# Optimization experiments

Measured on AMD Instinct MI355X. Metric: run time of the kernel, lower is better.

## Reference

```python
import jax, jax.numpy as jnp
import numpy as np

D_MODEL = 1024
NHEAD = 8
DPH = D_MODEL // NHEAD
DFF = 2048
EPS = 1e-5


def _layernorm(x, w, b):
    mu = jnp.mean(x, axis=-1, keepdims=True)
    var = jnp.mean((x - mu) ** 2, axis=-1, keepdims=True)
    return (x - mu) / jnp.sqrt(var + EPS) * w + b


def setup_inputs() -> dict:
    key = jax.random.key(0)
    ks = jax.random.split(key, 8)
    B, L = 8, 2048
    x = jax.random.normal(ks[0], (B, L, D_MODEL), dtype=jnp.float32)
    # HeadWiseLinear: per-head weight (nhead, dph, 4*dph), bias (nhead, 4*dph)
    ih_w = jax.random.normal(ks[1], (NHEAD, DPH, 4 * DPH), dtype=jnp.float32) * (1.0 / np.sqrt(DPH))
    # forget-gate bias init: linspace(3,6,d_model) in the f slot (second chunk), zeros elsewhere
    init_vals = jnp.linspace(3.0, 6.0, D_MODEL, dtype=jnp.float32).reshape(NHEAD, 1, DPH)
    init_vals = jnp.pad(init_vals, ((0, 0), (1, 2), (0, 0)))  # rows: i, f, z, o
    ih_b = init_vals.reshape(NHEAD, 4 * DPH)
    # linear_hh: Linear(dph, 4*dph, bias=False), stored as (dph, 4*dph) (x @ W)
    hh_w = jax.random.normal(ks[2], (DPH, 4 * DPH), dtype=jnp.float32) * (1.0 / np.sqrt(DPH))
    ln1_w = jnp.ones((D_MODEL,), jnp.float32); ln1_b = jnp.zeros((D_MODEL,), jnp.float32)
    ln2_w = jnp.ones((D_MODEL,), jnp.float32); ln2_b = jnp.zeros((D_MODEL,), jnp.float32)
    hn_w = jnp.ones((DPH,), jnp.float32); hn_b = jnp.zeros((DPH,), jnp.float32)
    ff_w1 = jax.random.normal(ks[3], (D_MODEL, 2 * DFF), dtype=jnp.float32) * (1.0 / np.sqrt(D_MODEL))
    ff_b1 = jnp.zeros((2 * DFF,), jnp.float32)
    ff_w2 = jax.random.normal(ks[4], (DFF, D_MODEL), dtype=jnp.float32) * (1.0 / np.sqrt(DFF))
    ff_b2 = jnp.zeros((D_MODEL,), jnp.float32)
    return dict(x=x, ih_w=ih_w, ih_b=ih_b, hh_w=hh_w, ln1_w=ln1_w, ln1_b=ln1_b,
                hn_w=hn_w, hn_b=hn_b, ln2_w=ln2_w, ln2_b=ln2_b,
                ff_w1=ff_w1, ff_b1=ff_b1, ff_w2=ff_w2, ff_b2=ff_b2)


def _slstm_core(x, ih_w, ih_b, hh_w, hn_w, hn_b):
    B, L, D = x.shape
    xh = x.reshape(B, L, NHEAD, DPH)
    # headwise input projection: (B,L,H,4*dph)
    proj = jnp.einsum('blhd,hdf->blhf', xh, ih_w) + ih_b
    proj = jnp.transpose(proj, (1, 0, 2, 3))  # (L,B,H,4*dph)

    h0 = jnp.zeros((B, NHEAD, DPH), x.dtype)
    c0 = jnp.zeros_like(h0)
    m0 = jnp.full_like(h0, -jnp.inf)  # stabilizer; matches scalar-0 first-step semantics
    n0 = jnp.zeros_like(h0)

    def step(carry, p_t):
        h, c, m, n = carry
        p = p_t + jnp.einsum('bhd,df->bhf', h, hh_w)
        i, f, z, o = jnp.split(p, 4, axis=-1)
        z = jnp.tanh(z)
        o = jax.nn.sigmoid(o)
        f = jax.nn.log_sigmoid(f) + m
        m_new = jnp.maximum(f, i)
        i_s = jnp.exp(i - m_new)
        f_s = jnp.exp(f - m_new)
        c = f_s * c + i_s * z
        n = f_s * n + i_s
        h = o * (c / n)
        return (h, c, m_new, n), h

    (h, c, _, _), out = jax.lax.scan(step, (h0, c0, m0, n0), proj)
    out = jnp.transpose(out, (1, 0, 2, 3))  # (B,L,H,dph)
    out = _layernorm(out, hn_w, hn_b)
    return out.reshape(B, L, D), (h, c)


def reference(x, ih_w, ih_b, hh_w, ln1_w, ln1_b, hn_w, hn_b, ln2_w, ln2_b,
              ff_w1, ff_b1, ff_w2, ff_b2):
    core_out, _ = _slstm_core(_layernorm(x, ln1_w, ln1_b), ih_w, ih_b, hh_w, hn_w, hn_b)
    y = core_out + x
    z = _layernorm(y, ln2_w, ln2_b)
    x12 = z @ ff_w1 + ff_b1
    x1, x2 = jnp.split(x12, 2, axis=-1)
    ff = (x1 * jax.nn.gelu(x2, approximate=False)) @ ff_w2 + ff_b2
    return ff + y
```

## Files before the change

kernel.cpp:

```cpp
#include <hip/hip_runtime.h>
#include <math.h>


#define D_MODEL 1024
#define NHEAD   8
#define DPH     128
#define DFF     2048
#define BATCH   8
#define SEQ     2048
#define NROWS   (BATCH * SEQ)
#define CHUNK_L 256
#define TGRP    32
#define ROWCH   8192
#define LN_EPS  1e-5f

typedef __attribute__((ext_vector_type(8))) short short8;
typedef __attribute__((ext_vector_type(4))) float f32x4;
typedef __attribute__((ext_vector_type(2))) _Float16 h2f;
typedef __attribute__((ext_vector_type(8))) _Float16 h8f;
union H8U { h8f v; h2f p[4]; };

#if __has_builtin(__builtin_amdgcn_fdot2)
#define DOT2(a, b, c) __builtin_amdgcn_fdot2((a), (b), (c), false)
#else
__device__ __forceinline__ float DOT2(h2f a, h2f b, float c) {
  return c + (float)a.x * (float)b.x + (float)a.y * (float)b.y;
}
#endif

__device__ __forceinline__ float qxor1(float v) {
#if __has_builtin(__builtin_amdgcn_update_dpp)
  union { float f; int i; } u; u.f = v;
  u.i = __builtin_amdgcn_update_dpp(u.i, u.i, 0xB1, 0xf, 0xf, true);
  return u.f;
#else
  return __shfl_xor(v, 1, 64);
#endif
}
__device__ __forceinline__ float qxor2(float v) {
#if __has_builtin(__builtin_amdgcn_update_dpp)
  union { float f; int i; } u; u.f = v;
  u.i = __builtin_amdgcn_update_dpp(u.i, u.i, 0x4E, 0xf, 0xf, true);
  return u.f;
#else
  return __shfl_xor(v, 2, 64);
#endif
}

__device__ __forceinline__ void gll16(const float* src, float* lds_base, int lane) {
#if __has_builtin(__builtin_amdgcn_global_load_lds)
  __builtin_amdgcn_global_load_lds(
      (const __attribute__((address_space(1))) unsigned int*)src,
      (__attribute__((address_space(3))) unsigned int*)lds_base, 16, 0, 0);
#else
  *(float4*)((char*)lds_base + lane * 16) = *(const float4*)src;
#endif
}

__device__ __forceinline__ float gelu_exact(float x) {
  return 0.5f * x * (1.0f + erff(x * 0.70710678118654752440f));
}

__device__ __forceinline__ unsigned short f2bf(float f) {
  union { float f; unsigned int u; } v; v.f = f;
  unsigned int r = v.u + 0x7fffu + ((v.u >> 16) & 1u);
  return (unsigned short)(r >> 16);
}

__device__ __forceinline__ float gate_step(float iv, float fv, float zraw, float oraw,
                                           float& c, float& nrm, float& m) {
  const float zv = 1.0f - 2.0f / (__expf(2.0f * zraw) + 1.0f);
  const float ov = 1.0f / (1.0f + __expf(-oraw));
  const float lf = fminf(fv, 0.0f) - __logf(1.0f + __expf(-fabsf(fv)));
  const float ft = lf + m;
  const float mn = fmaxf(ft, iv);
  const float is = __expf(iv - mn);
  const float fs = __expf(ft - mn);
  c = fs * c + is * zv;
  nrm = fs * nrm + is;
  m = mn;
  return ov * (c / nrm);
}

__global__ __launch_bounds__(256) void ln_stats_kernel(
    const float* __restrict__ in, float* __restrict__ mu_out,
    float* __restrict__ rs_out) {
  const int row = blockIdx.x, tid = threadIdx.x;
  const float4 v = ((const float4*)(in + (size_t)row * D_MODEL))[tid];
  float s  = v.x + v.y + v.z + v.w;
  float s2 = v.x*v.x + v.y*v.y + v.z*v.z + v.w*v.w;
  #pragma unroll
  for (int m = 1; m < 64; m <<= 1) { s += __shfl_xor(s, m, 64); s2 += __shfl_xor(s2, m, 64); }
  __shared__ float sa[4], sb[4];
  if ((tid & 63) == 0) { sa[tid >> 6] = s; sb[tid >> 6] = s2; }
  __syncthreads();
  if (tid == 0) {
    const float S  = sa[0] + sa[1] + sa[2] + sa[3];
    const float S2 = sb[0] + sb[1] + sb[2] + sb[3];
    const float mu = S * (1.0f / D_MODEL);
    const float var = S2 * (1.0f / D_MODEL) - mu * mu;
    mu_out[row] = mu;
    rs_out[row] = rsqrtf(var + LN_EPS);
  }
}

__global__ __launch_bounds__(256) void cvt_w(
    const float* __restrict__ src, short* __restrict__ dst, int K, int N) {
  __shared__ float tile[64][68];
  const int n0 = blockIdx.x * 64;
  const int k0 = blockIdx.y * 64;
  const int tid = threadIdx.x;
  #pragma unroll
  for (int i = 0; i < 16; ++i) {
    const int e = i * 256 + tid;
    const int kk = e >> 6, nn = e & 63;
    tile[kk][nn] = src[(size_t)(k0 + kk) * N + n0 + nn];
  }
  __syncthreads();
  #pragma unroll
  for (int i = 0; i < 2; ++i) {
    const int e = i * 256 + tid;
    const int nn = e >> 3, kc = (e & 7) * 8;
    short8 s;
    #pragma unroll
    for (int j = 0; j < 8; ++j) s[j] = (short)f2bf(tile[kc + j][nn]);
    *(short8*)(dst + (size_t)(n0 + nn) * K + k0 + kc) = s;
  }
}

__global__ __launch_bounds__(256) void cvt_hh(
    const float* __restrict__ hhw, h2f* __restrict__ hh2) {
  const int idx = blockIdx.x * 256 + threadIdx.x;
  const int k2 = idx >> 9, j = idx & 511;
  h2f v;
  v.x = (_Float16)hhw[(size_t)(2 * k2) * 512 + j];
  v.y = (_Float16)hhw[(size_t)(2 * k2 + 1) * 512 + j];
  hh2[idx] = v;
}

__global__ __launch_bounds__(256) void proj_gemm(
    const float* __restrict__ x, const float* __restrict__ mu1,
    const float* __restrict__ rs1, const float* __restrict__ ln1w,
    const float* __restrict__ ln1b, const float* __restrict__ ihw,
    const float* __restrict__ ihb, float* __restrict__ proj, int l0) {
  __shared__ __align__(16) float As[64][68];
  __shared__ __align__(16) float Bs[64][128];
  const int h  = blockIdx.z;
  const int n0 = blockIdx.y * 128;
  const int m0 = blockIdx.x * 64;
  const int tid = threadIdx.x;
  const int tm = (tid >> 5) << 3;
  const int tn = (tid & 31) << 2;
  float acc[8][4] = {};
  const float* Bb = ihw + (size_t)h * DPH * 512;
  for (int k0 = 0; k0 < DPH; k0 += 64) {
    #pragma unroll
    for (int i = 0; i < 4; ++i) {
      int idx = tid + i * 256;
      int r = idx >> 4, kk = (idx & 15) << 2;
      const int rowm = m0 + r;
      const int l = l0 + (rowm >> 3), b = rowm & 7;
      const int grow = b * SEQ + l;
      const float4 v = *(const float4*)(x + (size_t)grow * D_MODEL + h * DPH + k0 + kk);
      const float mu = mu1[grow], rs = rs1[grow];
      const float4 wv = *(const float4*)(ln1w + h * DPH + k0 + kk);
      const float4 bv = *(const float4*)(ln1b + h * DPH + k0 + kk);
      float4 o;
      o.x = (v.x - mu) * rs * wv.x + bv.x;
      o.y = (v.y - mu) * rs * wv.y + bv.y;
      o.z = (v.z - mu) * rs * wv.z + bv.z;
      o.w = (v.w - mu) * rs * wv.w + bv.w;
      *(float4*)&As[r][kk] = o;
    }
    #pragma unroll
    for (int i = 0; i < 8; ++i) {
      int idx = tid + i * 256;
      int kk = idx >> 5, nn = (idx & 31) << 2;
      *(float4*)&Bs[kk][nn] = *(const float4*)(Bb + (size_t)(k0 + kk) * 512 + n0 + nn);
    }
    __syncthreads();
    #pragma unroll 4
    for (int kk = 0; kk < 64; ++kk) {
      float a[8];
      #pragma unroll
      for (int i = 0; i < 8; ++i) a[i] = As[tm + i][kk];
      const float4 bv = *(const float4*)&Bs[kk][tn];
      #pragma unroll
      for (int i = 0; i < 8; ++i) {
        acc[i][0] += a[i] * bv.x; acc[i][1] += a[i] * bv.y;
        acc[i][2] += a[i] * bv.z; acc[i][3] += a[i] * bv.w;
      }
    }
    __syncthreads();
  }
  const float4 bias = *(const float4*)(ihb + h * 512 + n0 + tn);
  #pragma unroll
  for (int i = 0; i < 8; ++i) {
    const int rowm = m0 + tm + i;
    float4 o;
    o.x = acc[i][0] + bias.x; o.y = acc[i][1] + bias.y;
    o.z = acc[i][2] + bias.z; o.w = acc[i][3] + bias.w;
    *(float4*)(proj + ((size_t)rowm * NHEAD + h) * 512 + n0 + tn) = o;
  }
}

__global__ __launch_bounds__(512, 1) void scan_chunk(
    const float* __restrict__ proj, const h2f* __restrict__ hh2,
    float* __restrict__ state, float* __restrict__ hout, int l0) {
  const int bh = blockIdx.x, b = bh >> 3, h = bh & 7;
  const int tid = threadIdx.x;
  const int l = tid & 63, w = tid >> 6;
  const int q = l & 3, p = l >> 2;
  const int ch = 16 * w + p;
  __shared__ __align__(16) _Float16 h16[2][128];
  __shared__ __align__(16) float pbuf[2][TGRP][512];
  __shared__ __align__(16) float hstage[TGRP][128];

  h2f w2[4][16];
  #pragma unroll
  for (int j = 0; j < 4; ++j)
    #pragma unroll
    for (int kk = 0; kk < 16; ++kk)
      w2[j][kk] = hh2[(size_t)(16 * q + kk) * 512 + j * 128 + ch];

  float c, nrm, m;
  if (l0 == 0) {
    c = 0.0f; nrm = 0.0f; m = -1e30f;
    if (q == 0 && w == 0) { h16[0][p] = (_Float16)0.0f; }
    if (q == 0) h16[0][ch] = (_Float16)0.0f;
  } else {
    c   = state[bh * 128 + ch];
    nrm = state[8192  + bh * 128 + ch];
    m   = state[16384 + bh * 128 + ch];
    if (q == 0) h16[0][ch] = (_Float16)state[24576 + bh * 128 + ch];
  }

  const float* pbase = proj + (size_t)bh * 512;

  #define STAGE(NB, GR)                                                        \
    {                                                                          \
      _Pragma("unroll")                                                        \
      for (int i = 0; i < 8; ++i) {                                            \
        const int hr = i * 8 + w;                                              \
        const float* src = pbase + (size_t)((GR) * TGRP + (hr >> 1)) * 32768   \
                           + (hr & 1) * 256 + l * 4;                           \
        float* dst = &pbuf[NB][0][0] + hr * 256;                               \
        gll16(src, dst, l);                                                    \
      }                                                                        \
    }

  STAGE(0, 0)
  asm volatile("s_waitcnt vmcnt(0)" ::: "memory");
  __syncthreads();

  float hv = 0.0f;
  for (int t = 0; t < CHUNK_L; ++t) {
    const int tl = t & (TGRP - 1), gb = (t >> 5) & 1, cur = t & 1;
    if (tl == 0 && t + TGRP < CHUNK_L) STAGE(gb ^ 1, (t >> 5) + 1)
    float pa0 = 0.0f, pa1 = 0.0f, pa2 = 0.0f, pa3 = 0.0f;
    {
      const h8f* hp = (const h8f*)&h16[cur][q * 32];
      #pragma unroll
      for (int i = 0; i < 4; ++i) {
        H8U u; u.v = hp[i];
        #pragma unroll
        for (int e = 0; e < 4; ++e) {
          const int kk = i * 4 + e;
          pa0 = DOT2(u.p[e], w2[0][kk], pa0);
          pa1 = DOT2(u.p[e], w2[1][kk], pa1);
          pa2 = DOT2(u.p[e], w2[2][kk], pa2);
          pa3 = DOT2(u.p[e], w2[3][kk], pa3);
        }
      }
    }
    const float pv = pbuf[gb][tl][q * 128 + ch];
    pa0 += (q == 0) ? pv : 0.0f;
    pa1 += (q == 1) ? pv : 0.0f;
    pa2 += (q == 2) ? pv : 0.0f;
    pa3 += (q == 3) ? pv : 0.0f;
    pa0 += qxor1(pa0); pa1 += qxor1(pa1); pa2 += qxor1(pa2); pa3 += qxor1(pa3);
    pa0 += qxor2(pa0); pa1 += qxor2(pa1); pa2 += qxor2(pa2); pa3 += qxor2(pa3);
    hv = gate_step(pa0, pa1, pa2, pa3, c, nrm, m);
    if (q == 0) {
      h16[cur ^ 1][ch] = (_Float16)hv;
      hstage[tl][ch] = hv;
    }
    __syncthreads();
    if (tl == TGRP - 1) {
      const int s = tid >> 4, c8 = (tid & 15) << 3;
      const float4 v0 = *(const float4*)&hstage[s][c8];
      const float4 v1 = *(const float4*)&hstage[s][c8 + 4];
      float* dstp = hout + ((size_t)(b * SEQ + l0 + (t & ~(TGRP - 1)) + s)) * D_MODEL
                    + h * DPH + c8;
      *(float4*)dstp = v0;
      *(float4*)(dstp + 4) = v1;
      __syncthreads();
    }
  }

  if (q == 0) {
    state[bh * 128 + ch]          = c;
    state[8192  + bh * 128 + ch]  = nrm;
    state[16384 + bh * 128 + ch]  = m;
    state[24576 + bh * 128 + ch]  = hv;
  }
  #undef STAGE
}

__global__ __launch_bounds__(256) void post_kernel(
    float* __restrict__ yio, const float* __restrict__ x,
    const float* __restrict__ hnw, const float* __restrict__ hnb,
    float* __restrict__ mu2, float* __restrict__ rs2) {
  const int row = blockIdx.x, tid = threadIdx.x;
  const float4 hv = ((const float4*)(yio + (size_t)row * D_MODEL))[tid];
  float s  = hv.x + hv.y + hv.z + hv.w;
  float s2 = hv.x*hv.x + hv.y*hv.y + hv.z*hv.z + hv.w*hv.w;
  #pragma unroll
  for (int mm = 1; mm < 32; mm <<= 1) {
    s  += __shfl_xor(s,  mm, 32);
    s2 += __shfl_xor(s2, mm, 32);
  }
  const float mu = s * (1.0f / DPH);
  const float var = s2 * (1.0f / DPH) - mu * mu;
  const float rstd = rsqrtf(var + LN_EPS);
  const int dq = tid & 31;
  const float4 w4 = ((const float4*)hnw)[dq];
  const float4 b4 = ((const float4*)hnb)[dq];
  const float4 xv = ((const float4*)(x + (size_t)row * D_MODEL))[tid];
  float4 yv;
  yv.x = (hv.x - mu) * rstd * w4.x + b4.x + xv.x;
  yv.y = (hv.y - mu) * rstd * w4.y + b4.y + xv.y;
  yv.z = (hv.z - mu) * rstd * w4.z + b4.z + xv.z;
  yv.w = (hv.w - mu) * rstd * w4.w + b4.w + xv.w;
  ((float4*)(yio + (size_t)row * D_MODEL))[tid] = yv;
  float t1 = yv.x + yv.y + yv.z + yv.w;
  float t2 = yv.x*yv.x + yv.y*yv.y + yv.z*yv.z + yv.w*yv.w;
  #pragma unroll
  for (int mm = 1; mm < 64; mm <<= 1) {
    t1 += __shfl_xor(t1, mm, 64);
    t2 += __shfl_xor(t2, mm, 64);
  }
  __shared__ float sa[4], sb[4];
  if ((tid & 63) == 0) { sa[tid >> 6] = t1; sb[tid >> 6] = t2; }
  __syncthreads();
  if (tid == 0) {
    const float S  = sa[0] + sa[1] + sa[2] + sa[3];
    const float S2 = sb[0] + sb[1] + sb[2] + sb[3];
    const float m2 = S * (1.0f / D_MODEL);
    const float v2 = S2 * (1.0f / D_MODEL) - m2 * m2;
    mu2[row] = m2;
    rs2[row] = rsqrtf(v2 + LN_EPS);
  }
}

__global__ __launch_bounds__(256) void ff1_gemm(
    const float* __restrict__ y, const float* __restrict__ mu2,
    const float* __restrict__ rs2, const float* __restrict__ ln2w,
    const float* __restrict__ ln2b, const short* __restrict__ w1b,
    const float* __restrict__ b1, short* __restrict__ g, int row0) {
  __shared__ short As[128 * 64];
  __shared__ short Bs1[128 * 64];
  __shared__ short Bs2[128 * 64];
  const int tid = threadIdx.x;
  const int m0 = blockIdx.x * 128;
  const int n0 = blockIdx.y * 128;
  const int lane = tid & 63;
  const int wid = tid >> 6, wr = wid >> 1, wc = wid & 1;
  f32x4 acc1[4][4], acc2[4][4];
  #pragma unroll
  for (int i = 0; i < 4; ++i)
    #pragma unroll
    for (int j = 0; j < 4; ++j) { acc1[i][j] = (f32x4)0.0f; acc2[i][j] = (f32x4)0.0f; }
  for (int k0 = 0; k0 < D_MODEL; k0 += 64) {
    #pragma unroll
    for (int i = 0; i < 4; ++i) {
      const int cidx = tid + i * 256;
      const int r = cidx >> 3, c8 = cidx & 7;
      const int grow = row0 + m0 + r;
      const float* src = y + (size_t)grow * D_MODEL + k0 + c8 * 8;
      const float4 v0 = *(const float4*)src;
      const float4 v1 = *(const float4*)(src + 4);
      const float mu = mu2[grow], rs = rs2[grow];
      const float4 w0 = *(const float4*)(ln2w + k0 + c8 * 8);
      const float4 w1 = *(const float4*)(ln2w + k0 + c8 * 8 + 4);
      const float4 bb0 = *(const float4*)(ln2b + k0 + c8 * 8);
      const float4 bb1 = *(const float4*)(ln2b + k0 + c8 * 8 + 4);
      short8 s;
      s[0] = (short)f2bf((v0.x - mu) * rs * w0.x + bb0.x);
      s[1] = (short)f2bf((v0.y - mu) * rs * w0.y + bb0.y);
      s[2] = (short)f2bf((v0.z - mu) * rs * w0.z + bb0.z);
      s[3] = (short)f2bf((v0.w - mu) * rs * w0.w + bb0.w);
      s[4] = (short)f2bf((v1.x - mu) * rs * w1.x + bb1.x);
      s[5] = (short)f2bf((v1.y - mu) * rs * w1.y + bb1.y);
      s[6] = (short)f2bf((v1.z - mu) * rs * w1.z + bb1.z);
      s[7] = (short)f2bf((v1.w - mu) * rs * w1.w + bb1.w);
      *(short8*)&As[r * 64 + ((c8 ^ (r & 7)) << 3)] = s;
    }
    #pragma unroll
    for (int i = 0; i < 4; ++i) {
      const int cidx = tid + i * 256;
      const int r = cidx >> 3, c8 = cidx & 7;
      const short8 sv1 = *(const short8*)(w1b + (size_t)(n0 + r) * D_MODEL + k0 + c8 * 8);
      const short8 sv2 = *(const short8*)(w1b + (size_t)(DFF + n0 + r) * D_MODEL + k0 + c8 * 8);
      const int off = r * 64 + ((c8 ^ (r & 7)) << 3);
      *(short8*)&Bs1[off] = sv1;
      *(short8*)&Bs2[off] = sv2;
    }
    __syncthreads();
    #pragma unroll
    for (int ks = 0; ks < 2; ++ks) {
      short8 af[4], b1f[4], b2f[4];
      #pragma unroll
      for (int mf = 0; mf < 4; ++mf) {
        const int row = wr * 64 + mf * 16 + (lane & 15);
        const int c8 = ks * 4 + (lane >> 4);
        af[mf] = *(const short8*)&As[row * 64 + ((c8 ^ (row & 7)) << 3)];
      }
      #pragma unroll
      for (int nf = 0; nf < 4; ++nf) {
        const int row = wc * 64 + nf * 16 + (lane & 15);
        const int c8 = ks * 4 + (lane >> 4);
        const int off = row * 64 + ((c8 ^ (row & 7)) << 3);
        b1f[nf] = *(const short8*)&Bs1[off];
        b2f[nf] = *(const short8*)&Bs2[off];
      }
      #pragma unroll
      for (int mf = 0; mf < 4; ++mf)
        #pragma unroll
        for (int nf = 0; nf < 4; ++nf) {
          acc1[mf][nf] = __builtin_amdgcn_mfma_f32_16x16x32_bf16(af[mf], b1f[nf], acc1[mf][nf], 0, 0, 0);
          acc2[mf][nf] = __builtin_amdgcn_mfma_f32_16x16x32_bf16(af[mf], b2f[nf], acc2[mf][nf], 0, 0, 0);
        }
    }
    __syncthreads();
  }
  #pragma unroll
  for (int nf = 0; nf < 4; ++nf) {
    const int col = n0 + wc * 64 + nf * 16 + (lane & 15);
    const float bx1 = b1[col], bx2 = b1[DFF + col];
    #pragma unroll
    for (int mf = 0; mf < 4; ++mf) {
      const int rbase = m0 + wr * 64 + mf * 16 + ((lane >> 4) << 2);
      #pragma unroll
      for (int rr = 0; rr < 4; ++rr) {
        const float x1 = acc1[mf][nf][rr] + bx1;
        const float x2 = acc2[mf][nf][rr] + bx2;
        g[(size_t)(rbase + rr) * DFF + col] = (short)f2bf(x1 * gelu_exact(x2));
      }
    }
  }
}

__global__ __launch_bounds__(256) void ff2_gemm(
    const short* __restrict__ g, const short* __restrict__ w2b,
    const float* __restrict__ b2, float* __restrict__ out, int row0) {
  __shared__ short As[128 * 64];
  __shared__ short Bs[128 * 64];
  const int tid = threadIdx.x;
  const int m0 = blockIdx.x * 128;
  const int n0 = blockIdx.y * 128;
  const int lane = tid & 63;
  const int wid = tid >> 6, wr = wid >> 1, wc = wid & 1;
  f32x4 acc[4][4];
  #pragma unroll
  for (int i = 0; i < 4; ++i)
    #pragma unroll
    for (int j = 0; j < 4; ++j) acc[i][j] = (f32x4)0.0f;
  for (int k0 = 0; k0 < DFF; k0 += 64) {
    #pragma unroll
    for (int i = 0; i < 4; ++i) {
      const int cidx = tid + i * 256;
      const int r = cidx >> 3, c8 = cidx & 7;
      const int off = r * 64 + ((c8 ^ (r & 7)) << 3);
      *(short8*)&As[off] = *(const short8*)(g + (size_t)(m0 + r) * DFF + k0 + c8 * 8);
      *(short8*)&Bs[off] = *(const short8*)(w2b + (size_t)(n0 + r) * DFF + k0 + c8 * 8);
    }
    __syncthreads();
    #pragma unroll
    for (int ks = 0; ks < 2; ++ks) {
      short8 af[4], bf[4];
      #pragma unroll
      for (int mf = 0; mf < 4; ++mf) {
        const int row = wr * 64 + mf * 16 + (lane & 15);
        const int c8 = ks * 4 + (lane >> 4);
        af[mf] = *(const short8*)&As[row * 64 + ((c8 ^ (row & 7)) << 3)];
      }
      #pragma unroll
      for (int nf = 0; nf < 4; ++nf) {
        const int row = wc * 64 + nf * 16 + (lane & 15);
        const int c8 = ks * 4 + (lane >> 4);
        bf[nf] = *(const short8*)&Bs[row * 64 + ((c8 ^ (row & 7)) << 3)];
      }
      #pragma unroll
      for (int mf = 0; mf < 4; ++mf)
        #pragma unroll
        for (int nf = 0; nf < 4; ++nf)
          acc[mf][nf] = __builtin_amdgcn_mfma_f32_16x16x32_bf16(af[mf], bf[nf], acc[mf][nf], 0, 0, 0);
    }
    __syncthreads();
  }
  #pragma unroll
  for (int nf = 0; nf < 4; ++nf) {
    const int col = n0 + wc * 64 + nf * 16 + (lane & 15);
    const float bias = b2[col];
    #pragma unroll
    for (int mf = 0; mf < 4; ++mf) {
      const int rbase = row0 + m0 + wr * 64 + mf * 16 + ((lane >> 4) << 2);
      #pragma unroll
      for (int rr = 0; rr < 4; ++rr) {
        float* p = out + (size_t)(rbase + rr) * D_MODEL + col;
        *p = acc[mf][nf][rr] + bias + *p;
      }
    }
  }
}

extern "C" void kernel_launch(void* const* d_in, const int* in_sizes, int n_in,
                              void* d_out, int out_size, void* d_ws, size_t ws_size,
                              hipStream_t stream) {
  const float* x    = (const float*)d_in[0];
  const float* ihw  = (const float*)d_in[1];
  const float* ihb  = (const float*)d_in[2];
  const float* hhw  = (const float*)d_in[3];
  const float* ln1w = (const float*)d_in[4];
  const float* ln1b = (const float*)d_in[5];
  const float* hnw  = (const float*)d_in[6];
  const float* hnb  = (const float*)d_in[7];
  const float* ln2w = (const float*)d_in[8];
  const float* ln2b = (const float*)d_in[9];
  const float* ffw1 = (const float*)d_in[10];
  const float* ffb1 = (const float*)d_in[11];
  const float* ffw2 = (const float*)d_in[12];
  const float* ffb2 = (const float*)d_in[13];

  float* ws    = (float*)d_ws;
  float* r0    = ws;
  float* state = ws + 8388608;
  float* mu1   = ws + 8421376;
  float* rs1   = ws + 8437760;
  float* mu2   = ws + 8454144;
  float* rs2   = ws + 8470528;
  short* w1b   = (short*)(ws + 8486912);
  short* w2b   = (short*)(ws + 10584064);
  h2f*   hh2   = (h2f*)(ws + 11632640);
  short* gb    = (short*)r0;
  float* out   = (float*)d_out;

  cvt_w<<<dim3(4096 / 64, 1024 / 64), 256, 0, stream>>>(ffw1, w1b, 1024, 4096);
  cvt_w<<<dim3(1024 / 64, 2048 / 64), 256, 0, stream>>>(ffw2, w2b, 2048, 1024);
  cvt_hh<<<128, 256, 0, stream>>>(hhw, hh2);
  ln_stats_kernel<<<NROWS, 256, 0, stream>>>(x, mu1, rs1);
  for (int cidx = 0; cidx < SEQ / CHUNK_L; ++cidx) {
    const int l0 = cidx * CHUNK_L;
    proj_gemm<<<dim3(CHUNK_L * BATCH / 64, 512 / 128, NHEAD), 256, 0, stream>>>(
        x, mu1, rs1, ln1w, ln1b, ihw, ihb, r0, l0);
    scan_chunk<<<BATCH * NHEAD, 512, 0, stream>>>(r0, hh2, state, out, l0);
  }
  post_kernel<<<NROWS, 256, 0, stream>>>(out, x, hnw, hnb, mu2, rs2);
  for (int rc = 0; rc < NROWS / ROWCH; ++rc) {
    const int row0 = rc * ROWCH;
    ff1_gemm<<<dim3(ROWCH / 128, DFF / 128), 256, 0, stream>>>(
        out, mu2, rs2, ln2w, ln2b, w1b, ffb1, gb, row0);
    ff2_gemm<<<dim3(ROWCH / 128, D_MODEL / 128), 256, 0, stream>>>(
        gb, w2b, ffb2, out, row0);
  }
}
```

Before: 2.352 ms.

## Restructure sLSTM scan into unrolled groups with swizzled proj layout and fast reciprocals

```diff
diff --git a/kernel.cpp b/kernel.cpp
--- a/kernel.cpp
+++ b/kernel.cpp
@@ -10,7 +10,8 @@
 #define SEQ     2048
 #define NROWS   (BATCH * SEQ)
 #define CHUNK_L 256
-#define TGRP    32
+#define TGRP    16
+#define NGRP    (CHUNK_L / TGRP)
 #define ROWCH   8192
 #define LN_EPS  1e-5f
 
@@ -26,6 +27,12 @@
 __device__ __forceinline__ float DOT2(h2f a, h2f b, float c) {
   return c + (float)a.x * (float)b.x + (float)a.y * (float)b.y;
 }
+#endif
+
+#if __has_builtin(__builtin_amdgcn_rcpf)
+#define FRCP(x) __builtin_amdgcn_rcpf(x)
+#else
+#define FRCP(x) (1.0f / (x))
 #endif
 
 __device__ __forceinline__ float qxor1(float v) {
@@ -69,8 +76,8 @@
 
 __device__ __forceinline__ float gate_step(float iv, float fv, float zraw, float oraw,
                                            float& c, float& nrm, float& m) {
-  const float zv = 1.0f - 2.0f / (__expf(2.0f * zraw) + 1.0f);
-  const float ov = 1.0f / (1.0f + __expf(-oraw));
+  const float zv = 1.0f - 2.0f * FRCP(__expf(2.0f * zraw) + 1.0f);
+  const float ov = FRCP(1.0f + __expf(-oraw));
   const float lf = fminf(fv, 0.0f) - __logf(1.0f + __expf(-fabsf(fv)));
   const float ft = lf + m;
   const float mn = fmaxf(ft, iv);
@@ -79,7 +86,7 @@
   c = fs * c + is * zv;
   nrm = fs * nrm + is;
   m = mn;
-  return ov * (c / nrm);
+  return ov * c * FRCP(nrm);
 }
 
 __global__ __launch_bounds__(256) void ln_stats_kernel(
@@ -146,7 +153,8 @@
   __shared__ __align__(16) float As[64][68];
   __shared__ __align__(16) float Bs[64][128];
   const int h  = blockIdx.z;
-  const int n0 = blockIdx.y * 128;
+  const int qb = blockIdx.y;
+  const int n0 = qb * 128;
   const int m0 = blockIdx.x * 64;
   const int tid = threadIdx.x;
   const int tm = (tid >> 5) << 3;
@@ -194,13 +202,14 @@
     __syncthreads();
   }
   const float4 bias = *(const float4*)(ihb + h * 512 + n0 + tn);
+  const int pos = n0 + ((tn + 8 * qb) & 127);
   #pragma unroll
   for (int i = 0; i < 8; ++i) {
     const int rowm = m0 + tm + i;
     float4 o;
     o.x = acc[i][0] + bias.x; o.y = acc[i][1] + bias.y;
     o.z = acc[i][2] + bias.z; o.w = acc[i][3] + bias.w;
-    *(float4*)(proj + ((size_t)rowm * NHEAD + h) * 512 + n0 + tn) = o;
+    *(float4*)(proj + ((size_t)rowm * NHEAD + h) * 512 + pos) = o;
   }
 }
 
@@ -212,9 +221,10 @@
   const int l = tid & 63, w = tid >> 6;
   const int q = l & 3, p = l >> 2;
   const int ch = 16 * w + p;
+  const int pvoff = q * 128 + ((ch + 8 * q) & 127);
   __shared__ __align__(16) _Float16 h16[2][128];
   __shared__ __align__(16) float pbuf[2][TGRP][512];
-  __shared__ __align__(16) float hstage[TGRP][128];
+  __shared__ __align__(16) float hstage[2][TGRP][128];
 
   h2f w2[4][16];
   #pragma unroll
@@ -226,7 +236,6 @@
   float c, nrm, m;
   if (l0 == 0) {
     c = 0.0f; nrm = 0.0f; m = -1e30f;
-    if (q == 0 && w == 0) { h16[0][p] = (_Float16)0.0f; }
     if (q == 0) h16[0][ch] = (_Float16)0.0f;
   } else {
     c   = state[bh * 128 + ch];
@@ -240,7 +249,7 @@
   #define STAGE(NB, GR)                                                        \
     {                                                                          \
       _Pragma("unroll")                                                        \
-      for (int i = 0; i < 8; ++i) {                                            \
+      for (int i = 0; i < 4; ++i) {                                            \
         const int hr = i * 8 + w;                                              \
         const float* src = pbase + (size_t)((GR) * TGRP + (hr >> 1)) * 32768   \
                            + (hr & 1) * 256 + l * 4;                           \
@@ -254,47 +263,47 @@
   __syncthreads();
 
   float hv = 0.0f;
-  for (int t = 0; t < CHUNK_L; ++t) {
-    const int tl = t & (TGRP - 1), gb = (t >> 5) & 1, cur = t & 1;
-    if (tl == 0 && t + TGRP < CHUNK_L) STAGE(gb ^ 1, (t >> 5) + 1)
-    float pa0 = 0.0f, pa1 = 0.0f, pa2 = 0.0f, pa3 = 0.0f;
+  for (int grp = 0; grp < NGRP; ++grp) {
+    const int gb = grp & 1;
+    if (grp + 1 < NGRP) STAGE(gb ^ 1, grp + 1)
+    #pragma unroll
+    for (int tl = 0; tl < TGRP; ++tl) {
+      const int cur = tl & 1;
+      float pa0 = 0.0f, pa1 = 0.0f, pa2 = 0.0f, pa3 = 0.0f;
+      {
+        const h8f* hp = (const h8f*)&h16[cur][q * 32];
+        #pragma unroll
+        for (int i = 0; i < 4; ++i) {
+          H8U u; u.v = hp[i];
+          #pragma unroll
+          for (int e = 0; e < 4; ++e) {
+            const int kk = i * 4 + e;
+            pa0 = DOT2(u.p[e], w2[0][kk], pa0);
+            pa1 = DOT2(u.p[e], w2[1][kk], pa1);
+            pa2 = DOT2(u.p[e], w2[2][kk], pa2);
+            pa3 = DOT2(u.p[e], w2[3][kk], pa3);
+          }
+        }
+      }
+      const float pv = pbuf[gb][tl][pvoff];
+      pa0 += (q == 0) ? pv : 0.0f;
+      pa1 += (q == 1) ? pv : 0.0f;
+      pa2 += (q == 2) ? pv : 0.0f;
+      pa3 += (q == 3) ? pv : 0.0f;
+      pa0 += qxor1(pa0); pa1 += qxor1(pa1); pa2 += qxor1(pa2); pa3 += qxor1(pa3);
+      pa0 += qxor2(pa0); pa1 += qxor2(pa1); pa2 += qxor2(pa2); pa3 += qxor2(pa3);
+      hv = gate_step(pa0, pa1, pa2, pa3, c, nrm, m);
+      if (q == 0) {
+        h16[cur ^ 1][ch] = (_Float16)hv;
+        hstage[gb][tl][ch] = hv;
+      }
+      __syncthreads();
+    }
     {
-      const h8f* hp = (const h8f*)&h16[cur][q * 32];
-      #pragma unroll
-      for (int i = 0; i < 4; ++i) {
-        H8U u; u.v = hp[i];
-        #pragma unroll
-        for (int e = 0; e < 4; ++e) {
-          const int kk = i * 4 + e;
-          pa0 = DOT2(u.p[e], w2[0][kk], pa0);
-          pa1 = DOT2(u.p[e], w2[1][kk], pa1);
-          pa2 = DOT2(u.p[e], w2[2][kk], pa2);
-          pa3 = DOT2(u.p[e], w2[3][kk], pa3);
-        }
-      }
-    }
-    const float pv = pbuf[gb][tl][q * 128 + ch];
-    pa0 += (q == 0) ? pv : 0.0f;
-    pa1 += (q == 1) ? pv : 0.0f;
-    pa2 += (q == 2) ? pv : 0.0f;
-    pa3 += (q == 3) ? pv : 0.0f;
-    pa0 += qxor1(pa0); pa1 += qxor1(pa1); pa2 += qxor1(pa2); pa3 += qxor1(pa3);
-    pa0 += qxor2(pa0); pa1 += qxor2(pa1); pa2 += qxor2(pa2); pa3 += qxor2(pa3);
-    hv = gate_step(pa0, pa1, pa2, pa3, c, nrm, m);
-    if (q == 0) {
-      h16[cur ^ 1][ch] = (_Float16)hv;
-      hstage[tl][ch] = hv;
-    }
-    __syncthreads();
-    if (tl == TGRP - 1) {
-      const int s = tid >> 4, c8 = (tid & 15) << 3;
-      const float4 v0 = *(const float4*)&hstage[s][c8];
-      const float4 v1 = *(const float4*)&hstage[s][c8 + 4];
-      float* dstp = hout + ((size_t)(b * SEQ + l0 + (t & ~(TGRP - 1)) + s)) * D_MODEL
-                    + h * DPH + c8;
-      *(float4*)dstp = v0;
-      *(float4*)(dstp + 4) = v1;
-      __syncthreads();
+      const int s = tid >> 5, c8 = (tid & 31) << 2;
+      const float4 v0 = *(const float4*)&hstage[gb][s][c8];
+      *(float4*)(hout + ((size_t)(b * SEQ + l0 + grp * TGRP + s)) * D_MODEL
+                 + h * DPH + c8) = v0;
     }
   }
 
```

New measurement: 2.012 ms. 14.5% less time.
